# Kernel tuning notes

Hardware: AMD Instinct MI355X
Metric: run time of the kernel (lower is better)

## Reference

```python
import jax, jax.numpy as jnp
import numpy as np

E = 64       # expert_nums
D = 32       # embed_dim
H = 4        # num_heads
HD = D // H  # head_dim = 8
B = 524288
TOP_K = 2
NOISE_EPS = 0.01


def setup_inputs() -> dict:
    key = jax.random.key(0)
    ks = jax.random.split(key, 10)
    return {
        "taskID": jax.random.randint(ks[0], (B,), 0, 6),
        "embed_table": jax.random.normal(ks[1], (6, D), jnp.float32),
        "expert_keys": jax.random.normal(ks[2], (D, D), jnp.float32),
        "in_proj_w": jax.random.normal(ks[3], (3 * D, D), jnp.float32) * 0.1,
        "in_proj_b": jax.random.normal(ks[4], (3 * D,), jnp.float32) * 0.1,
        "fc_gate_w": jax.random.normal(ks[5], (E, D), jnp.float32) * 0.1,
        "fc_gate_b": jax.random.normal(ks[6], (E,), jnp.float32) * 0.1,
        "fc_noise_w": jax.random.normal(ks[7], (E, D), jnp.float32) * 0.1,
        "fc_noise_b": jax.random.normal(ks[8], (E,), jnp.float32) * 0.1,
        "noise": jax.random.normal(ks[9], (B, E), jnp.float32),
    }


def reference(taskID, embed_table, expert_keys, in_proj_w, in_proj_b,
              fc_gate_w, fc_gate_b, fc_noise_w, fc_noise_b, noise):
    bsz = taskID.shape[0]
    x = embed_table[taskID]                                   # [B, D] task embeddings (query)
    # nn.MultiheadAttention q/k projections (v and out_proj don't affect attn_weights)
    Wq, Wk = in_proj_w[:D], in_proj_w[D:2 * D]
    bq, bk = in_proj_b[:D], in_proj_b[D:2 * D]
    Q = (x @ Wq.T + bq).reshape(bsz, H, HD)                   # [B, H, HD]
    K = (expert_keys @ Wk.T + bk).reshape(D, H, HD)           # [S=32, H, HD], shared across batch
    scores = jnp.einsum('bhd,shd->bhs', Q, K) / np.sqrt(HD).astype(np.float32)
    attn_w = jax.nn.softmax(scores, axis=-1).mean(axis=1)     # averaged over heads -> [B, 32]
    expert_weight = jax.nn.softmax(attn_w, axis=-1)           # module re-applies softmax (faithful)
    clean_logits = expert_weight @ fc_gate_w.T + fc_gate_b    # [B, E]
    noise_std = jax.nn.softplus(expert_weight @ fc_noise_w.T + fc_noise_b) + NOISE_EPS
    logits = clean_logits + noise * noise_std                 # train=True path
    top_logits, top_indices = jax.lax.top_k(logits, min(TOP_K + 1, E))
    tk_logits = top_logits[:, :TOP_K]                         # [B, TOP_K]
    tk_indices = top_indices[:, :TOP_K]
    tk_gates = jax.nn.softmax(tk_logits, axis=-1)
    rows = jnp.arange(bsz)[:, None]
    gates = jnp.zeros_like(logits).at[rows, tk_indices].set(tk_gates)  # scatter sparse gates
    load = gates.sum(axis=0)                                  # [E]
    return gates, load
```

## Files before the change

### kernel.cpp

```cpp
#include <hip/hip_runtime.h>
#include <math.h>

#define NE 64
#define NTASK 6
#define BLK 256
#define GRID 1024
#define RPI 32

__global__ void precompute_kernel(
    const float* __restrict__ embed_table,
    const float* __restrict__ expert_keys,
    const float* __restrict__ in_proj_w,
    const float* __restrict__ in_proj_b,
    const float* __restrict__ fc_gate_w,
    const float* __restrict__ fc_gate_b,
    const float* __restrict__ fc_noise_w,
    const float* __restrict__ fc_noise_b,
    float*   __restrict__ tab_f,
    double2* __restrict__ tab_d,
    float*   __restrict__ load)
{
    __shared__ float s_win[96 * 32];
    __shared__ float s_wg[64 * 32];
    __shared__ float s_wn[64 * 32];
    __shared__ float s_keys[32 * 32];
    __shared__ float s_emb[6 * 32];
    __shared__ float s_bin[96], s_bg[64], s_bn[64];
    __shared__ double Ksh[32][32];
    __shared__ double Qsh[6][32];
    __shared__ double sc[24][32];
    __shared__ double attn[6][32];
    __shared__ double ew[6][32];
    __shared__ double red[24];
    __shared__ double red2[6];
    const int tid = threadIdx.x;

    if (tid < NE) load[tid] = 0.f;

    for (int i = tid; i < 96 * 32; i += BLK) s_win[i] = in_proj_w[i];
    for (int i = tid; i < 64 * 32; i += BLK) { s_wg[i] = fc_gate_w[i]; s_wn[i] = fc_noise_w[i]; }
    for (int i = tid; i < 32 * 32; i += BLK) s_keys[i] = expert_keys[i];
    for (int i = tid; i < 6 * 32;  i += BLK) s_emb[i] = embed_table[i];
    if (tid < 96) s_bin[tid] = in_proj_b[tid];
    if (tid < 64) { s_bg[tid] = fc_gate_b[tid]; s_bn[tid] = fc_noise_b[tid]; }
    __syncthreads();

    for (int idx = tid; idx < 32 * 32; idx += BLK) {
        int s = idx >> 5, j = idx & 31;
        double acc = (double)s_bin[32 + j];
        for (int d = 0; d < 32; ++d)
            acc += (double)s_keys[s * 32 + d] * (double)s_win[(32 + j) * 32 + d];
        Ksh[s][j] = acc;
    }
    for (int idx = tid; idx < NTASK * 32; idx += BLK) {
        int t = idx >> 5, j = idx & 31;
        double acc = (double)s_bin[j];
        for (int d = 0; d < 32; ++d)
            acc += (double)s_emb[t * 32 + d] * (double)s_win[j * 32 + d];
        Qsh[t][j] = acc;
    }
    __syncthreads();

    const double SCALE = 1.0 / (double)((float)2.8284271247461903);
    for (int idx = tid; idx < 24 * 32; idx += BLK) {
        int th = idx >> 5, s = idx & 31;
        int t = th >> 2, h = th & 3;
        double acc = 0.0;
        for (int d = 0; d < 8; ++d)
            acc += Qsh[t][h * 8 + d] * Ksh[s][h * 8 + d];
        sc[th][s] = acc * SCALE;
    }
    __syncthreads();
    if (tid < 24) {
        double m = sc[tid][0];
        for (int s = 1; s < 32; ++s) m = fmax(m, sc[tid][s]);
        red[tid] = m;
    }
    __syncthreads();
    for (int idx = tid; idx < 24 * 32; idx += BLK) {
        int th = idx >> 5, s = idx & 31;
        sc[th][s] = exp(sc[th][s] - red[th]);
    }
    __syncthreads();
    if (tid < 24) {
        double sum = 0.0;
        for (int s = 0; s < 32; ++s) sum += sc[tid][s];
        red[tid] = 1.0 / sum;
    }
    __syncthreads();
    for (int idx = tid; idx < NTASK * 32; idx += BLK) {
        int t = idx >> 5, s = idx & 31;
        attn[t][s] = 0.25 * (sc[t*4+0][s]*red[t*4+0] + sc[t*4+1][s]*red[t*4+1]
                           + sc[t*4+2][s]*red[t*4+2] + sc[t*4+3][s]*red[t*4+3]);
    }
    __syncthreads();
    if (tid < NTASK) {
        double m = attn[tid][0];
        for (int s = 1; s < 32; ++s) m = fmax(m, attn[tid][s]);
        red2[tid] = m;
    }
    __syncthreads();
    for (int idx = tid; idx < NTASK * 32; idx += BLK) {
        int t = idx >> 5, s = idx & 31;
        ew[t][s] = exp(attn[t][s] - red2[t]);
    }
    __syncthreads();
    if (tid < NTASK) {
        double sum = 0.0;
        for (int s = 0; s < 32; ++s) sum += ew[tid][s];
        red2[tid] = 1.0 / sum;
    }
    __syncthreads();

    {
        float2* tab_f2 = (float2*)tab_f;
        for (int idx = tid; idx < NTASK * NE; idx += BLK) {
            int t = idx >> 6, e = idx & 63;
            double inv = red2[t];
            double a  = (double)s_bg[e];
            double n0 = (double)s_bn[e];
            for (int d = 0; d < 32; ++d) {
                double w = ew[t][d] * inv;
                a  += w * (double)s_wg[e * 32 + d];
                n0 += w * (double)s_wn[e * 32 + d];
            }
            double sp = (n0 > 0.0) ? (n0 + log1p(exp(-n0))) : log1p(exp(n0));
            double ns = sp + 0.01;
            const int p  = e >> 1;
            const int cc = (p >> 3) & 3, rr = p & 7;
            const int i4 = t * 32 + p;
            const int dst = (i4 & ~7) | (rr ^ ((2 * cc + t) & 7));
            tab_f2[dst * 2 + (e & 1)] = make_float2((float)a, (float)ns);
            tab_d[t * 64 + e] = make_double2(a, ns);
        }
        for (int idx = NTASK * NE + tid; idx < 512; idx += BLK) {
            tab_f2[idx] = make_float2(0.f, 0.f);
        }
    }
}

__global__ __launch_bounds__(BLK) void router_kernel(
    const int*     __restrict__ taskID,
    const float4*  __restrict__ noise4,
    const float4*  __restrict__ tabf4,
    const double2* __restrict__ tabd,
    float* __restrict__ gates,
    float* __restrict__ load,
    int B)
{
    __shared__ float4  s_tabf4[256];
    __shared__ double2 s_tabd[512];
    __shared__ float   s_load[NE];

    const int tid = threadIdx.x;
    for (int i = tid; i < 256; i += BLK) s_tabf4[i] = tabf4[i];
    for (int i = tid; i < 512; i += BLK) s_tabd[i] = tabd[i];
    if (tid < NE) s_load[tid] = 0.f;
    __syncthreads();

    const int lane  = tid & 63;
    const int sub   = lane >> 2;
    const int c     = lane & 3;
    const int ebase = c * 16;
    const int W = (blockIdx.x * BLK + tid) >> 6;
    const int nWaves = GRID * (BLK / 64);
    const int nGroup = (B + RPI - 1) / RPI;
    const float4 zero4 = make_float4(0.f, 0.f, 0.f, 0.f);

    int   tcA = 0, tcB = 0;
    float4 a0, a1, a2, a3, a4, a5, a6, a7;
    a0=a1=a2=a3=a4=a5=a6=a7 = zero4;
    bool okA = false, okB = false;
    int  rowA = 0, rowB = 0;

    if (W < nGroup) {
        rowA = W * RPI + sub;       okA = rowA < B;
        rowB = W * RPI + 16 + sub;  okB = rowB < B;
        if (okA) {
            tcA = taskID[rowA];
            const int nb = rowA * 16 + c * 4;
            a0 = noise4[nb+0]; a1 = noise4[nb+1]; a2 = noise4[nb+2]; a3 = noise4[nb+3];
        }
        if (okB) {
            tcB = taskID[rowB];
            const int nb = rowB * 16 + c * 4;
            a4 = noise4[nb+0]; a5 = noise4[nb+1]; a6 = noise4[nb+2]; a7 = noise4[nb+3];
        }
    }

    for (int g = W; g < nGroup; g += nWaves) {
        const int gn = g + nWaves;
        int   tnA = 0, tnB = 0;
        float4 b0, b1, b2, b3, b4, b5, b6, b7;
        b0=b1=b2=b3=b4=b5=b6=b7 = zero4;
        bool oknA = false, oknB = false;
        int  rownA = 0, rownB = 0;
        if (gn < nGroup) {
            rownA = gn * RPI + sub;       oknA = rownA < B;
            rownB = gn * RPI + 16 + sub;  oknB = rownB < B;
            if (oknA) {
                tnA = taskID[rownA];
                const int nb = rownA * 16 + c * 4;
                b0 = noise4[nb+0]; b1 = noise4[nb+1]; b2 = noise4[nb+2]; b3 = noise4[nb+3];
            }
            if (oknB) {
                tnB = taskID[rownB];
                const int nb = rownB * 16 + c * 4;
                b4 = noise4[nb+0]; b5 = noise4[nb+1]; b6 = noise4[nb+2]; b7 = noise4[nb+3];
            }
        }

#define INS2(l_, e_, n_) {                                                     \
        const bool b1_ = (l_) > v1, b2_ = (l_) > v2;                           \
        v2 = b1_ ? v1 : (b2_ ? (l_) : v2);                                     \
        i2 = b1_ ? i1 : (b2_ ? (e_) : i2);                                     \
        n2 = b1_ ? n1 : (b2_ ? (n_) : n2);                                     \
        v1 = b1_ ? (l_) : v1;                                                  \
        i1 = b1_ ? (e_) : i1;                                                  \
        n1 = b1_ ? (n_) : n1; }

#define STEP(r_, nlo_, nhi_) {                                                 \
        const float4 tv = s_tabf4[tb + ((r_) ^ x)];                            \
        const float l0 = __fadd_rn(tv.x, __fmul_rn((nlo_), tv.y));             \
        const float l1 = __fadd_rn(tv.z, __fmul_rn((nhi_), tv.w));             \
        INS2(l0, ebase + 2 * (r_),     (nlo_));                                \
        INS2(l1, ebase + 2 * (r_) + 1, (nhi_)); }

#define PROCESS(t_, ok_, row_, z0, z1, z2, z3)                                 \
    {                                                                          \
        const int t  = (t_);                                                   \
        const int x  = (2 * c + t) & 7;                                        \
        const int tb = t * 32 + c * 8;                                         \
        float v1 = -INFINITY, v2 = -INFINITY;                                  \
        int   i1 = 0, i2 = 0;                                                  \
        float n1 = 0.f, n2 = 0.f;                                              \
        STEP(0, z0.x, z0.y); STEP(1, z0.z, z0.w);                              \
        STEP(2, z1.x, z1.y); STEP(3, z1.z, z1.w);                              \
        STEP(4, z2.x, z2.y); STEP(5, z2.z, z2.w);                              \
        STEP(6, z3.x, z3.y); STEP(7, z3.z, z3.w);                              \
        _Pragma("unroll")                                                      \
        for (int m = 1; m <= 2; m <<= 1) {                                     \
            const float w1 = __shfl_xor(v1, m), w2 = __shfl_xor(v2, m);        \
            const int   j1 = __shfl_xor(i1, m), j2 = __shfl_xor(i2, m);        \
            const float q1 = __shfl_xor(n1, m), q2 = __shfl_xor(n2, m);        \
            const bool aw = (v1 > w1) || (v1 == w1 && i1 < j1);                \
            const float p1 = aw ? v1 : w1, p2 = aw ? v2 : w2;                  \
            const int   pi1 = aw ? i1 : j1, pi2 = aw ? i2 : j2;                \
            const float pn1 = aw ? n1 : q1, pn2 = aw ? n2 : q2;                \
            const float u1 = aw ? w1 : v1;                                     \
            const int   ui1 = aw ? j1 : i1;                                    \
            const float un1 = aw ? q1 : n1;                                    \
            const bool b2 = (p2 > u1) || (p2 == u1 && pi2 < ui1);              \
            v1 = p1;  i1 = pi1; n1 = pn1;                                      \
            v2 = b2 ? p2 : u1;  i2 = b2 ? pi2 : ui1;  n2 = b2 ? pn2 : un1;     \
        }                                                                      \
        const double2 A  = s_tabd[t * 64 + i1];                                \
        const double2 Bt = s_tabd[t * 64 + i2];                                \
        double da = A.x  + (double)n1 * A.y;  int ia = i1;                     \
        double db = Bt.x + (double)n2 * Bt.y; int ib = i2;                     \
        if (db > da || (db == da && ib < ia)) {                                \
            double tv_ = da; da = db; db = tv_;                                \
            int ti_ = ia; ia = ib; ib = ti_;                                   \
        }                                                                      \
        const float e2 = expf((float)(db - da));                               \
        const float g1 = 1.0f / (1.0f + e2);                                   \
        const float g2 = e2 / (1.0f + e2);                                     \
        if (ok_) {                                                             \
            float* grow = gates + (size_t)(row_) * 64;                         \
            float4* g4 = reinterpret_cast<float4*>(grow + ebase);              \
            g4[0] = zero4; g4[1] = zero4; g4[2] = zero4; g4[3] = zero4;        \
            if ((ia >> 4) == c) grow[ia] = g1;                                 \
            if ((ib >> 4) == c) grow[ib] = g2;                                 \
            if (c == 0) {                                                      \
                atomicAdd(&s_load[ia], g1);                                    \
                atomicAdd(&s_load[ib], g2);                                    \
            }                                                                  \
        }                                                                      \
    }

        PROCESS(tcA, okA, rowA, a0, a1, a2, a3)
        PROCESS(tcB, okB, rowB, a4, a5, a6, a7)

#undef PROCESS
#undef STEP
#undef INS2

        tcA = tnA; rowA = rownA; okA = oknA;
        tcB = tnB; rowB = rownB; okB = oknB;
        a0 = b0; a1 = b1; a2 = b2; a3 = b3;
        a4 = b4; a5 = b5; a6 = b6; a7 = b7;
    }
    __syncthreads();
    if (tid < NE) atomicAdd(&load[tid], s_load[tid]);
}

extern "C" void kernel_launch(void* const* d_in, const int* in_sizes, int n_in,
                              void* d_out, int out_size, void* d_ws, size_t ws_size,
                              hipStream_t stream) {
    const int*   taskID      = (const int*)  d_in[0];
    const float* embed_table = (const float*)d_in[1];
    const float* expert_keys = (const float*)d_in[2];
    const float* in_proj_w   = (const float*)d_in[3];
    const float* in_proj_b   = (const float*)d_in[4];
    const float* fc_gate_w   = (const float*)d_in[5];
    const float* fc_gate_b   = (const float*)d_in[6];
    const float* fc_noise_w  = (const float*)d_in[7];
    const float* fc_noise_b  = (const float*)d_in[8];
    const float* noise       = (const float*)d_in[9];

    const int B = in_sizes[0];

    float*   tab_f = (float*)d_ws;
    double2* tab_d = (double2*)((char*)d_ws + 4096);

    float* gates = (float*)d_out;
    float* load  = gates + (size_t)B * NE;

    precompute_kernel<<<1, BLK, 0, stream>>>(embed_table, expert_keys, in_proj_w, in_proj_b,
                                             fc_gate_w, fc_gate_b, fc_noise_w, fc_noise_b,
                                             tab_f, tab_d, load);

    router_kernel<<<GRID, BLK, 0, stream>>>(taskID, (const float4*)noise,
                                            (const float4*)tab_f, tab_d,
                                            gates, load, B);
}
```

Baseline: 117.7 us.

## Coalesce noise loads and gate stores via LDS transpose and shuffle broadcast

Noise is now loaded so that consecutive lanes read consecutive float4s (fully coalesced), then transposed through a swizzled per-wave LDS staging buffer into the per-row layout the top-k logic needs. Gate rows are written as contiguous float4s, with each lane rebuilding its chunk from the winner indices and gates broadcast by shuffle, replacing strided zero stores plus scattered scalar writes. This aims to improve memory access efficiency on a bandwidth-bound kernel, at the cost of extra LDS traffic, shuffles and 16KB more shared memory per block.

Result: no change. 119.6 us (+1.6%).

```diff
diff --git a/kernel.cpp b/kernel.cpp
--- a/kernel.cpp
+++ b/kernel.cpp
@@ -144,13 +144,14 @@
     const float4*  __restrict__ noise4,
     const float4*  __restrict__ tabf4,
     const double2* __restrict__ tabd,
-    float* __restrict__ gates,
-    float* __restrict__ load,
+    float4* __restrict__ gates4,
+    float*  __restrict__ load,
     int B)
 {
     __shared__ float4  s_tabf4[256];
     __shared__ double2 s_tabd[512];
     __shared__ float   s_load[NE];
+    __shared__ float4  s_stage[BLK/64][256];
 
     const int tid = threadIdx.x;
     for (int i = tid; i < 256; i += BLK) s_tabf4[i] = tabf4[i];
@@ -159,55 +160,46 @@
     __syncthreads();
 
     const int lane  = tid & 63;
+    const int wid   = tid >> 6;
     const int sub   = lane >> 2;
     const int c     = lane & 3;
     const int ebase = c * 16;
     const int W = (blockIdx.x * BLK + tid) >> 6;
     const int nWaves = GRID * (BLK / 64);
     const int nGroup = (B + RPI - 1) / RPI;
+    const int n4 = B * 16;
     const float4 zero4 = make_float4(0.f, 0.f, 0.f, 0.f);
 
-    int   tcA = 0, tcB = 0;
-    float4 a0, a1, a2, a3, a4, a5, a6, a7;
-    a0=a1=a2=a3=a4=a5=a6=a7 = zero4;
-    bool okA = false, okB = false;
-    int  rowA = 0, rowB = 0;
-
-    if (W < nGroup) {
-        rowA = W * RPI + sub;       okA = rowA < B;
-        rowB = W * RPI + 16 + sub;  okB = rowB < B;
-        if (okA) {
-            tcA = taskID[rowA];
-            const int nb = rowA * 16 + c * 4;
-            a0 = noise4[nb+0]; a1 = noise4[nb+1]; a2 = noise4[nb+2]; a3 = noise4[nb+3];
-        }
-        if (okB) {
-            tcB = taskID[rowB];
-            const int nb = rowB * 16 + c * 4;
-            a4 = noise4[nb+0]; a5 = noise4[nb+1]; a6 = noise4[nb+2]; a7 = noise4[nb+3];
-        }
+    float4 cur[8], nxt[8];
+    int tA = 0, tB = 0;
+
+    {
+        const int gb = W * 512;
+        #pragma unroll
+        for (int j = 0; j < 8; ++j) {
+            const int idx = gb + j * 64 + lane;
+            cur[j] = (W < nGroup && idx < n4) ? noise4[idx] : zero4;
+        }
+        const int rA = W * RPI + sub, rB = rA + 16;
+        tA = (W < nGroup && rA < B) ? taskID[rA] : 0;
+        tB = (W < nGroup && rB < B) ? taskID[rB] : 0;
     }
 
     for (int g = W; g < nGroup; g += nWaves) {
         const int gn = g + nWaves;
-        int   tnA = 0, tnB = 0;
-        float4 b0, b1, b2, b3, b4, b5, b6, b7;
-        b0=b1=b2=b3=b4=b5=b6=b7 = zero4;
-        bool oknA = false, oknB = false;
-        int  rownA = 0, rownB = 0;
-        if (gn < nGroup) {
-            rownA = gn * RPI + sub;       oknA = rownA < B;
-            rownB = gn * RPI + 16 + sub;  oknB = rownB < B;
-            if (oknA) {
-                tnA = taskID[rownA];
-                const int nb = rownA * 16 + c * 4;
-                b0 = noise4[nb+0]; b1 = noise4[nb+1]; b2 = noise4[nb+2]; b3 = noise4[nb+3];
+        {
+            const int gb = gn * 512;
+            #pragma unroll
+            for (int j = 0; j < 8; ++j) {
+                const int idx = gb + j * 64 + lane;
+                nxt[j] = (gn < nGroup && idx < n4) ? noise4[idx] : zero4;
             }
-            if (oknB) {
-                tnB = taskID[rownB];
-                const int nb = rownB * 16 + c * 4;
-                b4 = noise4[nb+0]; b5 = noise4[nb+1]; b6 = noise4[nb+2]; b7 = noise4[nb+3];
-            }
+        }
+        int ntA = 0, ntB = 0;
+        {
+            const int rA = gn * RPI + sub, rB = rA + 16;
+            ntA = (gn < nGroup && rA < B) ? taskID[rA] : 0;
+            ntB = (gn < nGroup && rB < B) ? taskID[rB] : 0;
         }
 
 #define INS2(l_, e_, n_) {                                                     \
@@ -226,18 +218,31 @@
         INS2(l0, ebase + 2 * (r_),     (nlo_));                                \
         INS2(l1, ebase + 2 * (r_) + 1, (nhi_)); }
 
-#define PROCESS(t_, ok_, row_, z0, z1, z2, z3)                                 \
+#define PROCHALF(t_, rowbase_, cj0, cj1, cj2, cj3)                             \
     {                                                                          \
+                         \
+        _Pragma("unroll")                                                      \
+        for (int j = 0; j < 4; ++j) {                                          \
+            const float4 vsrc = (j == 0) ? (cj0) : (j == 1) ? (cj1)            \
+                              : (j == 2) ? (cj2) : (cj3);                      \
+            const int f  = j * 64 + lane;                                      \
+            const int rl = f >> 4, q = f & 15;                                 \
+            s_stage[wid][rl * 16 + (q ^ rl)] = vsrc;                           \
+        }                                                                      \
+        float4 z[4];                                                           \
+        _Pragma("unroll")                                                      \
+        for (int k = 0; k < 4; ++k)                                            \
+            z[k] = s_stage[wid][sub * 16 + ((c * 4 + k) ^ sub)];               \
         const int t  = (t_);                                                   \
         const int x  = (2 * c + t) & 7;                                        \
         const int tb = t * 32 + c * 8;                                         \
         float v1 = -INFINITY, v2 = -INFINITY;                                  \
         int   i1 = 0, i2 = 0;                                                  \
         float n1 = 0.f, n2 = 0.f;                                              \
-        STEP(0, z0.x, z0.y); STEP(1, z0.z, z0.w);                              \
-        STEP(2, z1.x, z1.y); STEP(3, z1.z, z1.w);                              \
-        STEP(4, z2.x, z2.y); STEP(5, z2.z, z2.w);                              \
-        STEP(6, z3.x, z3.y); STEP(7, z3.z, z3.w);                              \
+        STEP(0, z[0].x, z[0].y); STEP(1, z[0].z, z[0].w);                      \
+        STEP(2, z[1].x, z[1].y); STEP(3, z[1].z, z[1].w);                      \
+        STEP(4, z[2].x, z[2].y); STEP(5, z[2].z, z[2].w);                      \
+        STEP(6, z[3].x, z[3].y); STEP(7, z[3].z, z[3].w);                      \
         _Pragma("unroll")                                                      \
         for (int m = 1; m <= 2; m <<= 1) {                                     \
             const float w1 = __shfl_xor(v1, m), w2 = __shfl_xor(v2, m);        \
@@ -265,30 +270,44 @@
         const float e2 = expf((float)(db - da));                               \
         const float g1 = 1.0f / (1.0f + e2);                                   \
         const float g2 = e2 / (1.0f + e2);                                     \
-        if (ok_) {                                                             \
-            float* grow = gates + (size_t)(row_) * 64;                         \
-            float4* g4 = reinterpret_cast<float4*>(grow + ebase);              \
-            g4[0] = zero4; g4[1] = zero4; g4[2] = zero4; g4[3] = zero4;        \
-            if ((ia >> 4) == c) grow[ia] = g1;                                 \
-            if ((ib >> 4) == c) grow[ib] = g2;                                 \
-            if (c == 0) {                                                      \
-                atomicAdd(&s_load[ia], g1);                                    \
-                atomicAdd(&s_load[ib], g2);                                    \
-            }                                                                  \
-        }                                                                      \
-    }
-
-        PROCESS(tcA, okA, rowA, a0, a1, a2, a3)
-        PROCESS(tcB, okB, rowB, a4, a5, a6, a7)
-
-#undef PROCESS
+        const int iab = ia | (ib << 8);                                        \
+        if (c == 0 && ((rowbase_) + sub) < B) {                                \
+            atomicAdd(&s_load[ia], g1);                                        \
+            atomicAdd(&s_load[ib], g2);                                        \
+        }                                                                      \
+         \
+        const int gb_ = (rowbase_) * 16;                                       \
+        _Pragma("unroll")                                                      \
+        for (int j = 0; j < 4; ++j) {                                          \
+            const int f  = j * 64 + lane;                                      \
+            const int rr = f >> 4;                                             \
+            const int p  = f & 15;                                             \
+            const int src = rr << 2;                                           \
+            const int   siab = __shfl(iab, src);                               \
+            const float sg1  = __shfl(g1,  src);                               \
+            const float sg2  = __shfl(g2,  src);                               \
+            const int sia = siab & 255, sib = siab >> 8;                       \
+            const int e0 = p * 4;                                              \
+            float4 w;                                                          \
+            w.x = (e0 + 0 == sia) ? sg1 : ((e0 + 0 == sib) ? sg2 : 0.f);       \
+            w.y = (e0 + 1 == sia) ? sg1 : ((e0 + 1 == sib) ? sg2 : 0.f);       \
+            w.z = (e0 + 2 == sia) ? sg1 : ((e0 + 2 == sib) ? sg2 : 0.f);       \
+            w.w = (e0 + 3 == sia) ? sg1 : ((e0 + 3 == sib) ? sg2 : 0.f);       \
+            const int gidx = gb_ + f;                                          \
+            if (gidx < n4) gates4[gidx] = w;                                   \
+        }                                                                      \
+    }
+
+        PROCHALF(tA, g * RPI,      cur[0], cur[1], cur[2], cur[3])
+        PROCHALF(tB, g * RPI + 16, cur[4], cur[5], cur[6], cur[7])
+
+#undef PROCHALF
 #undef STEP
 #undef INS2
 
-        tcA = tnA; rowA = rownA; okA = oknA;
-        tcB = tnB; rowB = rownB; okB = oknB;
-        a0 = b0; a1 = b1; a2 = b2; a3 = b3;
-        a4 = b4; a5 = b5; a6 = b6; a7 = b7;
+        #pragma unroll
+        for (int j = 0; j < 8; ++j) cur[j] = nxt[j];
+        tA = ntA; tB = ntB;
     }
     __syncthreads();
     if (tid < NE) atomicAdd(&load[tid], s_load[tid]);
@@ -322,5 +341,5 @@
 
     router_kernel<<<GRID, BLK, 0, stream>>>(taskID, (const float4*)noise,
                                             (const float4*)tab_f, tab_d,
-                                            gates, load, B);
+                                            (float4*)gates, load, B);
 }
```
